# Performance work log

Hardware: AMD Instinct MI355X
Metric: run time of the kernel (lower is better)

Reference implementation:

```python
import jax, jax.numpy as jnp
import numpy as np

N_NODES = 100000


def _gcn_conv(x, W, b, src, dst, deg_inv_sqrt, n):
    # PyG GCNConv: h = x @ W; out[i] = sum_{(j->i)} norm_ji * h[j] + b
    h = x @ W                                   # [N, out_dim]
    norm = deg_inv_sqrt[src] * deg_inv_sqrt[dst]  # [E_total]
    msg = h[src] * norm[:, None]                # gather + scale
    out = jax.ops.segment_sum(msg, dst, num_segments=n)  # scatter-add
    return out + b


def setup_inputs() -> dict:
    key = jax.random.key(0)
    k1, k2, k3, k4, k5, k6 = jax.random.split(key, 6)
    num_features, hidden, embedding_size = 128, 32, 64
    n_edges = 3200000
    x = jax.random.normal(k1, (N_NODES, num_features), dtype=jnp.float32)
    edge_index = jax.random.randint(k2, (2, n_edges), 0, N_NODES, dtype=jnp.int64)
    # Glorot init like PyG GCNConv
    W1 = jax.random.normal(k3, (num_features, hidden), dtype=jnp.float32) * (1.0 / np.sqrt(num_features))
    b1 = jnp.zeros((hidden,), dtype=jnp.float32)
    W2 = jax.random.normal(k4, (hidden, embedding_size), dtype=jnp.float32) * (1.0 / np.sqrt(hidden))
    b2 = jnp.zeros((embedding_size,), dtype=jnp.float32)
    return {"x": x, "edge_index": edge_index, "W1": W1, "b1": b1, "W2": W2, "b2": b2}


def reference(x, edge_index, W1, b1, W2, b2):
    n = x.shape[0]
    # add self-loops (GCNConv default add_self_loops=True)
    loop = jnp.arange(n, dtype=edge_index.dtype)
    src = jnp.concatenate([edge_index[0], loop])
    dst = jnp.concatenate([edge_index[1], loop])
    # symmetric normalization: deg includes self-loops, edge_weight = 1
    deg = jax.ops.segment_sum(jnp.ones_like(dst, dtype=x.dtype), dst, num_segments=n)
    deg_inv_sqrt = jnp.where(deg > 0, jax.lax.rsqrt(deg), 0.0)

    h = _gcn_conv(x, W1, b1, src, dst, deg_inv_sqrt, n)
    h = jax.nn.relu(h)
    # F.dropout(p=0.2, training=False) -> identity in eval mode
    out = _gcn_conv(h, W2, b2, src, dst, deg_inv_sqrt, n)
    return out
```

## Files before the change

kernel.cpp:

```cpp
#include <hip/hip_runtime.h>
#include <hip/hip_bf16.h>


#define NF 128
#define HID 32
#define EMB 64

#define BSHIFT 10
#define BNODES 1024
#define CAP 36864
#define NBUKMAX 128
#define TILE 4096
#define EPT 16
#define CHUNKS 8

typedef float vf4 __attribute__((ext_vector_type(4)));

static __device__ __forceinline__ unsigned bf16rne(float f) {
    unsigned u = __float_as_uint(f);
    return (u + 0x7fffu + ((u >> 16) & 1u)) >> 16;
}

static __device__ __host__ __forceinline__ int hslot(int b, int c) {
    return ((b >> 3) << 6) | (c << 3) | (b & 7);
}

#define ACC8(v) \
    a0 += __uint_as_float((v).x << 16); a1 += __uint_as_float((v).x & 0xffff0000u); \
    a2 += __uint_as_float((v).y << 16); a3 += __uint_as_float((v).y & 0xffff0000u); \
    a4 += __uint_as_float((v).z << 16); a5 += __uint_as_float((v).z & 0xffff0000u); \
    a6 += __uint_as_float((v).w << 16); a7 += __uint_as_float((v).w & 0xffff0000u);

__global__ void k_detect(const unsigned* __restrict__ raw, int* __restrict__ flag) {
    int t = blockIdx.x * blockDim.x + threadIdx.x;
    unsigned w = raw[2 * t + 1];
    if (w != 0u) atomicOr(flag, 1);
}

__global__ __launch_bounds__(256) void k_part(const void* __restrict__ ei,
                                              const int* __restrict__ flag,
                                              unsigned* __restrict__ pairs,
                                              int* __restrict__ bcur,
                                              int* __restrict__ cnt_ovf,
                                              unsigned long long* __restrict__ ovf,
                                              int* __restrict__ ovfcnt,
                                              int E, int nbuk) {
    __shared__ unsigned sEnt[TILE];
    __shared__ unsigned char sB[TILE];
    __shared__ int hcnt[NBUKMAX], lstart[NBUKMAX], gbase[NBUKMAX], lcur[NBUKMAX];
    const int tid = threadIdx.x;
    const int tile0 = blockIdx.x * TILE;
    if (tile0 >= E) return;
    const int tcnt = min(TILE, E - tile0);
    const bool is64 = (*flag == 0);

    for (int b = tid; b < nbuk; b += 256) { hcnt[b] = 0; lcur[b] = 0; }
    __syncthreads();

    int ms[EPT], md[EPT];
#pragma unroll
    for (int k = 0; k < EPT; ++k) {
        int i = tile0 + k * 256 + tid;
        ms[k] = -1;
        if (i < tile0 + tcnt) {
            int s, d;
            if (is64) {
                const long long* p = (const long long*)ei;
                s = (int)__builtin_nontemporal_load(&p[i]);
                d = (int)__builtin_nontemporal_load(&p[(size_t)E + i]);
            } else {
                const int* p = (const int*)ei;
                s = __builtin_nontemporal_load(&p[i]);
                d = __builtin_nontemporal_load(&p[E + i]);
            }
            ms[k] = s; md[k] = d;
            atomicAdd(&hcnt[d >> BSHIFT], 1);
        }
    }
    __syncthreads();

    if (tid < 64) {
        int i0 = tid * 2, i1 = tid * 2 + 1;
        int c0 = (i0 < nbuk) ? hcnt[i0] : 0;
        int c1 = (i1 < nbuk) ? hcnt[i1] : 0;
        int run = c0 + c1, inc = run;
#pragma unroll
        for (int off = 1; off < 64; off <<= 1) {
            int t2 = __shfl_up(inc, off);
            if (tid >= off) inc += t2;
        }
        int excl = inc - run;
        if (i0 < nbuk) { lstart[i0] = excl;      gbase[i0] = c0 ? atomicAdd(&bcur[i0], c0) : 0; }
        if (i1 < nbuk) { lstart[i1] = excl + c0; gbase[i1] = c1 ? atomicAdd(&bcur[i1], c1) : 0; }
    }
    __syncthreads();

#pragma unroll
    for (int k = 0; k < EPT; ++k) {
        if (ms[k] >= 0) {
            int b = md[k] >> BSHIFT;
            int c = atomicAdd(&lcur[b], 1);
            int slot = lstart[b] + c;
            sEnt[slot] = ((unsigned)(md[k] & (BNODES - 1)) << 17) | (unsigned)ms[k];
            sB[slot] = (unsigned char)b;
        }
    }
    __syncthreads();

    for (int j = tid; j < tcnt; j += 256) {
        unsigned ent = sEnt[j];
        int b = sB[j];
        int g = gbase[b] + (j - lstart[b]);
        if (g < CAP) {
            pairs[(size_t)b * CAP + g] = ent;
        } else {
            int d = (b << BSHIFT) | (int)(ent >> 17);
            int s = (int)(ent & 0x1FFFFu);
            int o = atomicAdd(ovfcnt, 1);
            ovf[o] = ((unsigned long long)(unsigned)d << 32) | (unsigned)s;
            atomicAdd(&cnt_ovf[d], 1);
        }
    }
}

__global__ void k_bscan(const int* __restrict__ bcur, int* __restrict__ bbase,
                        int* __restrict__ roff, int nbuk, int E, int N) {
    __shared__ int sh[128];
    int t = threadIdx.x;
    int v = (t < nbuk) ? bcur[t] : 0;
    sh[t] = v;
    __syncthreads();
    for (int off = 1; off < 128; off <<= 1) {
        int add = (t >= off) ? sh[t - off] : 0;
        __syncthreads();
        sh[t] += add;
        __syncthreads();
    }
    if (t < nbuk) bbase[t] = sh[t] - v;
    if (t == 0) roff[N] = E;
}

__global__ __launch_bounds__(256) void k_hist(const unsigned* __restrict__ pairs,
                                              const int* __restrict__ bcur,
                                              int* __restrict__ histc, int nbuk) {
    __shared__ int hist[BNODES];
    const int idx = blockIdx.x;
    const int c = (idx >> 3) & 7;
    const int b = (idx & 7) | ((idx >> 6) << 3);
    if (b >= nbuk) return;
    const int tid = threadIdx.x;
    const int nb = min(bcur[b], CAP);
    const int csz = (nb + CHUNKS - 1) / CHUNKS;
    const int i0 = c * csz, i1 = min(nb, i0 + csz);
    const unsigned* pp = pairs + (size_t)b * CAP;
    for (int i = tid; i < BNODES; i += 256) hist[i] = 0;
    __syncthreads();
    for (int i = i0 + tid; i < i1; i += 256)
        atomicAdd(&hist[__builtin_nontemporal_load(&pp[i]) >> 17], 1);
    __syncthreads();
    int* out = histc + ((size_t)idx << 10);
    for (int i = tid; i < BNODES; i += 256) out[i] = hist[i];
}

__global__ __launch_bounds__(256) void k_nscan(int* __restrict__ histc,
                                               const int* __restrict__ bbase,
                                               const int* __restrict__ cnt_ovf,
                                               int* __restrict__ roff,
                                               int* __restrict__ cursor,
                                               float* __restrict__ dis, int N) {
    __shared__ int part[256];
    const int b = blockIdx.x, tid = threadIdx.x;
    const int base = bbase[b];
    int h[4][CHUNKS], stg[4], tv[4];
    int run = 0;
    const int l0 = tid * 4;
#pragma unroll
    for (int k = 0; k < 4; ++k) {
        int l = l0 + k;
        int node = (b << BSHIFT) + l;
        int st = 0;
#pragma unroll
        for (int c = 0; c < CHUNKS; ++c) {
            h[k][c] = histc[((size_t)hslot(b, c) << 10) + l];
            st += h[k][c];
        }
        stg[k] = st;
        int ov = (node < N) ? cnt_ovf[node] : 0;
        tv[k] = st + ov;
        run += tv[k];
    }
    part[tid] = run;
    __syncthreads();
    for (int off = 1; off < 256; off <<= 1) {
        int add = (tid >= off) ? part[tid - off] : 0;
        __syncthreads();
        part[tid] += add;
        __syncthreads();
    }
    int excl = part[tid] - run;
#pragma unroll
    for (int k = 0; k < 4; ++k) {
        int l = l0 + k;
        int node = (b << BSHIFT) + l;
        if (node < N) {
            roff[node] = base + excl;
            cursor[node] = base + excl + stg[k];
            dis[node] = rsqrtf((float)(tv[k] + 1));
        }
        int cb = base + excl;
#pragma unroll
        for (int c = 0; c < CHUNKS; ++c) {
            int hh = h[k][c];
            histc[((size_t)hslot(b, c) << 10) + l] = cb;
            cb += hh;
        }
        excl += tv[k];
    }
}

__global__ __launch_bounds__(256) void k_scat2(const unsigned* __restrict__ pairs,
                                               const int* __restrict__ bcur,
                                               const int* __restrict__ histc,
                                               int* __restrict__ csr, int nbuk) {
    __shared__ int cbase[BNODES];
    __shared__ int lc[BNODES];
    const int idx = blockIdx.x;
    const int c = (idx >> 3) & 7;
    const int b = (idx & 7) | ((idx >> 6) << 3);
    if (b >= nbuk) return;
    const int tid = threadIdx.x;
    const int nb = min(bcur[b], CAP);
    const int csz = (nb + CHUNKS - 1) / CHUNKS;
    const int i0 = c * csz, i1 = min(nb, i0 + csz);
    const unsigned* pp = pairs + (size_t)b * CAP;
    const int* hc = histc + ((size_t)idx << 10);
    for (int i = tid; i < BNODES; i += 256) { cbase[i] = hc[i]; lc[i] = 0; }
    __syncthreads();
    for (int i = i0 + tid; i < i1; i += 256) {
        unsigned ent = pp[i];
        int l = ent >> 17;
        int pos = cbase[l] + atomicAdd(&lc[l], 1);
        csr[pos] = (int)(ent & 0x1FFFFu);
    }
}

__global__ __launch_bounds__(256) void k_ovf(const unsigned long long* __restrict__ ovf,
                                             const int* __restrict__ ovfcnt,
                                             int* __restrict__ cursor,
                                             int* __restrict__ csr) {
    int n = *ovfcnt;
    for (int i = blockIdx.x * 256 + threadIdx.x; i < n; i += 256 * 8) {
        unsigned long long pr = ovf[i];
        int pos = atomicAdd(&cursor[(int)(unsigned)(pr >> 32)], 1);
        csr[pos] = (int)(unsigned)pr;
    }
}

__global__ __launch_bounds__(256) void k_gemm1(const float* __restrict__ x,
                                               const float* __restrict__ W,
                                               const float* __restrict__ dis,
                                               unsigned* __restrict__ h1b, int N) {
    __shared__ float sW[NF * HID];
    __shared__ float sx[32][132];
    const int t = threadIdx.x;
    for (int i = t; i < NF * HID; i += 256) sW[i] = W[i];
    const int row0 = blockIdx.x * 32;
    {
        const float4* xv = (const float4*)(x + (size_t)row0 * NF);
        for (int i = t; i < 32 * 32; i += 256) {
            int r = i >> 5, c = i & 31;
            float4 v = make_float4(0.f, 0.f, 0.f, 0.f);
            if (row0 + r < N) v = xv[(size_t)r * 32 + c];
            *(float4*)&sx[r][c * 4] = v;
        }
    }
    __syncthreads();
    const int col4 = (t & 7) * 4;
    const int row = t >> 3;
    float a0 = 0.f, a1 = 0.f, a2 = 0.f, a3 = 0.f;
#pragma unroll 8
    for (int k = 0; k < NF; ++k) {
        float xs = sx[row][k];
        float4 w = *(const float4*)&sW[k * HID + col4];
        a0 += xs * w.x; a1 += xs * w.y; a2 += xs * w.z; a3 += xs * w.w;
    }
    int r = row0 + row;
    if (r < N) {
        float d = dis[r];
        unsigned u0 = bf16rne(a0 * d) | (bf16rne(a1 * d) << 16);
        unsigned u1 = bf16rne(a2 * d) | (bf16rne(a3 * d) << 16);
        *(uint2*)&h1b[(size_t)r * 16 + (t & 7) * 2] = make_uint2(u0, u1);
    }
}

__global__ __launch_bounds__(256) void k_agg1(const uint4* __restrict__ h1b,
                                              const int* __restrict__ roff,
                                              const int* __restrict__ csr,
                                              const float* __restrict__ dis,
                                              const float* __restrict__ b1,
                                              uint4* __restrict__ t_out, int N) {
    int tt = blockIdx.x * 256 + threadIdx.x;
    int node = tt >> 2;
    if (node >= N) return;
    int j = tt & 3;
    uint4 u = h1b[(size_t)node * 4 + j];
    float a0, a1, a2, a3, a4, a5, a6, a7;
    a0 = __uint_as_float(u.x << 16); a1 = __uint_as_float(u.x & 0xffff0000u);
    a2 = __uint_as_float(u.y << 16); a3 = __uint_as_float(u.y & 0xffff0000u);
    a4 = __uint_as_float(u.z << 16); a5 = __uint_as_float(u.z & 0xffff0000u);
    a6 = __uint_as_float(u.w << 16); a7 = __uint_as_float(u.w & 0xffff0000u);
    int e0 = roff[node], e1 = roff[node + 1];
    int e = e0;
    for (; e + 4 <= e1; e += 4) {
        int s0 = __builtin_nontemporal_load(&csr[e + 0]);
        int s1 = __builtin_nontemporal_load(&csr[e + 1]);
        int s2 = __builtin_nontemporal_load(&csr[e + 2]);
        int s3 = __builtin_nontemporal_load(&csr[e + 3]);
        uint4 v0 = h1b[(size_t)s0 * 4 + j];
        uint4 v1 = h1b[(size_t)s1 * 4 + j];
        uint4 v2 = h1b[(size_t)s2 * 4 + j];
        uint4 v3 = h1b[(size_t)s3 * 4 + j];
        ACC8(v0) ACC8(v1) ACC8(v2) ACC8(v3)
    }
    for (; e < e1; ++e) {
        int s = __builtin_nontemporal_load(&csr[e]);
        uint4 v = h1b[(size_t)s * 4 + j];
        ACC8(v)
    }
    float d = dis[node];
    float4 bb0 = *(const float4*)&b1[j * 8];
    float4 bb1 = *(const float4*)&b1[j * 8 + 4];
    float r0 = fmaxf(a0 * d + bb0.x, 0.f) * d, r1 = fmaxf(a1 * d + bb0.y, 0.f) * d;
    float r2 = fmaxf(a2 * d + bb0.z, 0.f) * d, r3 = fmaxf(a3 * d + bb0.w, 0.f) * d;
    float r4 = fmaxf(a4 * d + bb1.x, 0.f) * d, r5 = fmaxf(a5 * d + bb1.y, 0.f) * d;
    float r6 = fmaxf(a6 * d + bb1.z, 0.f) * d, r7 = fmaxf(a7 * d + bb1.w, 0.f) * d;
    uint4 o;
    o.x = bf16rne(r0) | (bf16rne(r1) << 16);
    o.y = bf16rne(r2) | (bf16rne(r3) << 16);
    o.z = bf16rne(r4) | (bf16rne(r5) << 16);
    o.w = bf16rne(r6) | (bf16rne(r7) << 16);
    t_out[(size_t)node * 4 + j] = o;
}

__global__ __launch_bounds__(256) void k_agg2(const uint4* __restrict__ tb,
                                              const int* __restrict__ roff,
                                              const int* __restrict__ csr,
                                              const float* __restrict__ dis,
                                              float* __restrict__ s2, int N) {
    int tt = blockIdx.x * 256 + threadIdx.x;
    int node = tt >> 2;
    if (node >= N) return;
    int j = tt & 3;
    uint4 u = tb[(size_t)node * 4 + j];
    float a0, a1, a2, a3, a4, a5, a6, a7;
    a0 = __uint_as_float(u.x << 16); a1 = __uint_as_float(u.x & 0xffff0000u);
    a2 = __uint_as_float(u.y << 16); a3 = __uint_as_float(u.y & 0xffff0000u);
    a4 = __uint_as_float(u.z << 16); a5 = __uint_as_float(u.z & 0xffff0000u);
    a6 = __uint_as_float(u.w << 16); a7 = __uint_as_float(u.w & 0xffff0000u);
    int e0 = roff[node], e1 = roff[node + 1];
    int e = e0;
    for (; e + 4 <= e1; e += 4) {
        int s0 = __builtin_nontemporal_load(&csr[e + 0]);
        int s1 = __builtin_nontemporal_load(&csr[e + 1]);
        int s2i = __builtin_nontemporal_load(&csr[e + 2]);
        int s3 = __builtin_nontemporal_load(&csr[e + 3]);
        uint4 v0 = tb[(size_t)s0 * 4 + j];
        uint4 v1 = tb[(size_t)s1 * 4 + j];
        uint4 v2 = tb[(size_t)s2i * 4 + j];
        uint4 v3 = tb[(size_t)s3 * 4 + j];
        ACC8(v0) ACC8(v1) ACC8(v2) ACC8(v3)
    }
    for (; e < e1; ++e) {
        int s = __builtin_nontemporal_load(&csr[e]);
        uint4 v = tb[(size_t)s * 4 + j];
        ACC8(v)
    }
    float d = dis[node];
    float* op = &s2[(size_t)node * HID + j * 8];
    *(float4*)op       = make_float4(a0 * d, a1 * d, a2 * d, a3 * d);
    *(float4*)(op + 4) = make_float4(a4 * d, a5 * d, a6 * d, a7 * d);
}

__global__ __launch_bounds__(256) void k_gemm2(const float* __restrict__ a,
                                               const float* __restrict__ W,
                                               const float* __restrict__ b2,
                                               float* __restrict__ out, int N) {
    __shared__ float sW[HID * EMB];
    __shared__ float sx[32][36];
    const int t = threadIdx.x;
    for (int i = t; i < HID * EMB; i += 256) sW[i] = W[i];
    const int row0 = blockIdx.x * 32;
    {
        const float4* av = (const float4*)(a + (size_t)row0 * HID);
        int r = t >> 3, c = t & 7;
        float4 v = make_float4(0.f, 0.f, 0.f, 0.f);
        if (row0 + r < N) v = av[(size_t)r * 8 + c];
        *(float4*)&sx[r][c * 4] = v;
    }
    __syncthreads();
    const int col4 = (t & 15) * 4;
    const int r0 = t >> 4;
    float a00 = 0.f, a01 = 0.f, a02 = 0.f, a03 = 0.f;
    float a10 = 0.f, a11 = 0.f, a12 = 0.f, a13 = 0.f;
#pragma unroll
    for (int k = 0; k < HID; ++k) {
        float4 w = *(const float4*)&sW[k * EMB + col4];
        float xa = sx[r0][k];
        float xb = sx[r0 + 16][k];
        a00 += xa * w.x; a01 += xa * w.y; a02 += xa * w.z; a03 += xa * w.w;
        a10 += xb * w.x; a11 += xb * w.y; a12 += xb * w.z; a13 += xb * w.w;
    }
    float4 bb = *(const float4*)&b2[col4];
    int ra = row0 + r0, rb = row0 + r0 + 16;
    if (ra < N) {
        vf4 o; o.x = a00 + bb.x; o.y = a01 + bb.y; o.z = a02 + bb.z; o.w = a03 + bb.w;
        __builtin_nontemporal_store(o, (vf4*)&out[(size_t)ra * EMB + col4]);
    }
    if (rb < N) {
        vf4 o; o.x = a10 + bb.x; o.y = a11 + bb.y; o.z = a12 + bb.z; o.w = a13 + bb.w;
        __builtin_nontemporal_store(o, (vf4*)&out[(size_t)rb * EMB + col4]);
    }
}

extern "C" void kernel_launch(void* const* d_in, const int* in_sizes, int n_in,
                              void* d_out, int out_size, void* d_ws, size_t ws_size,
                              hipStream_t stream) {
    const float* x  = (const float*)d_in[0];
    const void*  ei = d_in[1];
    const float* W1 = (const float*)d_in[2];
    const float* b1 = (const float*)d_in[3];
    const float* W2 = (const float*)d_in[4];
    const float* b2 = (const float*)d_in[5];
    float* out = (float*)d_out;

    const int N = in_sizes[0] / NF;
    const int E = in_sizes[1] / 2;
    const int nbuk = (N + BNODES - 1) >> BSHIFT;

    char* ws = (char*)d_ws;
    size_t off = 0;
    auto take = [&](size_t bytes) -> void* {
        void* p = ws + off;
        off += (bytes + 255) & ~(size_t)255;
        return p;
    };
    int* cnt_ovf = (int*)take((size_t)N * 4);
    int* bcur    = (int*)take((size_t)NBUKMAX * 4);
    int* ovfcnt  = (int*)take(4);
    int* flag    = (int*)take(4);
    size_t zbytes = off;
    int*                bbase  = (int*)take((size_t)NBUKMAX * 4);
    int*                roff   = (int*)take((size_t)(N + 1) * 4);
    int*                cursor = (int*)take((size_t)N * 4);
    float*              dis    = (float*)take((size_t)N * 4);
    int*                histc  = (int*)take((size_t)NBUKMAX * CHUNKS * BNODES * 4);
    unsigned*           pairs  = (unsigned*)take((size_t)nbuk * CAP * 4);
    unsigned long long* ovf    = (unsigned long long*)take((size_t)E * 8);
    int*                csr    = (int*)take((size_t)E * 4);
    unsigned*           h1b    = (unsigned*)take((size_t)N * HID * 2);
    unsigned*           tb     = (unsigned*)take((size_t)N * HID * 2);
    float*              s2     = (float*)take((size_t)N * HID * 4);

    (void)hipMemsetAsync(cnt_ovf, 0, zbytes, stream);

    const int gridBC = ((nbuk + 7) / 8) * 64;

    k_detect<<<16, 256, 0, stream>>>((const unsigned*)ei, flag);
    k_part<<<(E + TILE - 1) / TILE, 256, 0, stream>>>(ei, flag, pairs, bcur, cnt_ovf,
                                                      ovf, ovfcnt, E, nbuk);
    k_bscan<<<1, 128, 0, stream>>>(bcur, bbase, roff, nbuk, E, N);
    k_hist<<<gridBC, 256, 0, stream>>>(pairs, bcur, histc, nbuk);
    k_nscan<<<nbuk, 256, 0, stream>>>(histc, bbase, cnt_ovf, roff, cursor, dis, N);
    k_scat2<<<gridBC, 256, 0, stream>>>(pairs, bcur, histc, csr, nbuk);
    k_ovf<<<8, 256, 0, stream>>>(ovf, ovfcnt, cursor, csr);

    k_gemm1<<<(N + 31) / 32, 256, 0, stream>>>(x, W1, dis, h1b, N);
    k_agg1<<<((size_t)N * 4 + 255) / 256, 256, 0, stream>>>((const uint4*)h1b, roff, csr,
                                                            dis, b1, (uint4*)tb, N);
    k_agg2<<<((size_t)N * 4 + 255) / 256, 256, 0, stream>>>((const uint4*)tb, roff, csr,
                                                            dis, s2, N);
    k_gemm2<<<(N + 31) / 32, 256, 0, stream>>>(s2, W2, b2, out, N);
}
```

Before: 252.5 us.

## Fold dtype detection into partition, per-wave histograms, and unroll gather loops

Removes the separate dtype-detect kernel and does the int32/int64 check inside each partition block. The shared-memory bucket histogram is split per wavefront to reduce atomic contention. The CSR scatter loop is unrolled by four and both aggregation loops by eight to raise memory-level parallelism. The layer-2 aggregation output uses nontemporal stores. The cost is more shared memory and registers, and the detection is now per tile rather than global.

```diff
diff --git a/kernel.cpp b/kernel.cpp
--- a/kernel.cpp
+++ b/kernel.cpp
@@ -15,6 +15,7 @@
 #define CHUNKS 8
 
 typedef float vf4 __attribute__((ext_vector_type(4)));
+typedef unsigned vu4 __attribute__((ext_vector_type(4)));
 
 static __device__ __forceinline__ unsigned bf16rne(float f) {
     unsigned u = __float_as_uint(f);
@@ -31,14 +32,7 @@
     a4 += __uint_as_float((v).z << 16); a5 += __uint_as_float((v).z & 0xffff0000u); \
     a6 += __uint_as_float((v).w << 16); a7 += __uint_as_float((v).w & 0xffff0000u);
 
-__global__ void k_detect(const unsigned* __restrict__ raw, int* __restrict__ flag) {
-    int t = blockIdx.x * blockDim.x + threadIdx.x;
-    unsigned w = raw[2 * t + 1];
-    if (w != 0u) atomicOr(flag, 1);
-}
-
 __global__ __launch_bounds__(256) void k_part(const void* __restrict__ ei,
-                                              const int* __restrict__ flag,
                                               unsigned* __restrict__ pairs,
                                               int* __restrict__ bcur,
                                               int* __restrict__ cnt_ovf,
@@ -47,15 +41,31 @@
                                               int E, int nbuk) {
     __shared__ unsigned sEnt[TILE];
     __shared__ unsigned char sB[TILE];
-    __shared__ int hcnt[NBUKMAX], lstart[NBUKMAX], gbase[NBUKMAX], lcur[NBUKMAX];
+    __shared__ int hcntw[4][NBUKMAX];
+    __shared__ int lcurw[4][NBUKMAX];
+    __shared__ int lstart[NBUKMAX], gbase[NBUKMAX];
+    __shared__ int sNZ;
     const int tid = threadIdx.x;
+    const int w = tid >> 6;
     const int tile0 = blockIdx.x * TILE;
     if (tile0 >= E) return;
     const int tcnt = min(TILE, E - tile0);
-    const bool is64 = (*flag == 0);
-
-    for (int b = tid; b < nbuk; b += 256) { hcnt[b] = 0; lcur[b] = 0; }
-    __syncthreads();
+
+    if (tid == 0) sNZ = 0;
+    for (int b = tid; b < 4 * NBUKMAX; b += 256) {
+        ((int*)hcntw)[b] = 0;
+        ((int*)lcurw)[b] = 0;
+    }
+    __syncthreads();
+    {
+        int i = tile0 + tid;
+        if (i < E) {
+            unsigned hw = ((const unsigned*)ei)[2 * (size_t)i + 1];
+            if (hw) sNZ = 1;
+        }
+    }
+    __syncthreads();
+    const bool is64 = (sNZ == 0);
 
     int ms[EPT], md[EPT];
 #pragma unroll
@@ -74,15 +84,16 @@
                 d = __builtin_nontemporal_load(&p[E + i]);
             }
             ms[k] = s; md[k] = d;
-            atomicAdd(&hcnt[d >> BSHIFT], 1);
+            atomicAdd(&hcntw[w][d >> BSHIFT], 1);
         }
     }
     __syncthreads();
 
     if (tid < 64) {
         int i0 = tid * 2, i1 = tid * 2 + 1;
-        int c0 = (i0 < nbuk) ? hcnt[i0] : 0;
-        int c1 = (i1 < nbuk) ? hcnt[i1] : 0;
+        int c0 = 0, c1 = 0;
+        if (i0 < nbuk) { c0 = hcntw[0][i0] + hcntw[1][i0] + hcntw[2][i0] + hcntw[3][i0]; }
+        if (i1 < nbuk) { c1 = hcntw[0][i1] + hcntw[1][i1] + hcntw[2][i1] + hcntw[3][i1]; }
         int run = c0 + c1, inc = run;
 #pragma unroll
         for (int off = 1; off < 64; off <<= 1) {
@@ -90,8 +101,20 @@
             if (tid >= off) inc += t2;
         }
         int excl = inc - run;
-        if (i0 < nbuk) { lstart[i0] = excl;      gbase[i0] = c0 ? atomicAdd(&bcur[i0], c0) : 0; }
-        if (i1 < nbuk) { lstart[i1] = excl + c0; gbase[i1] = c1 ? atomicAdd(&bcur[i1], c1) : 0; }
+        if (i0 < nbuk) {
+            lstart[i0] = excl;
+            gbase[i0] = c0 ? atomicAdd(&bcur[i0], c0) : 0;
+            int off2 = excl;
+#pragma unroll
+            for (int ww = 0; ww < 4; ++ww) { int t3 = hcntw[ww][i0]; hcntw[ww][i0] = off2; off2 += t3; }
+        }
+        if (i1 < nbuk) {
+            lstart[i1] = excl + c0;
+            gbase[i1] = c1 ? atomicAdd(&bcur[i1], c1) : 0;
+            int off2 = excl + c0;
+#pragma unroll
+            for (int ww = 0; ww < 4; ++ww) { int t3 = hcntw[ww][i1]; hcntw[ww][i1] = off2; off2 += t3; }
+        }
     }
     __syncthreads();
 
@@ -99,8 +122,7 @@
     for (int k = 0; k < EPT; ++k) {
         if (ms[k] >= 0) {
             int b = md[k] >> BSHIFT;
-            int c = atomicAdd(&lcur[b], 1);
-            int slot = lstart[b] + c;
+            int slot = hcntw[w][b] + atomicAdd(&lcurw[w][b], 1);
             sEnt[slot] = ((unsigned)(md[k] & (BNODES - 1)) << 17) | (unsigned)ms[k];
             sB[slot] = (unsigned char)b;
         }
@@ -158,8 +180,8 @@
     for (int i = i0 + tid; i < i1; i += 256)
         atomicAdd(&hist[__builtin_nontemporal_load(&pp[i]) >> 17], 1);
     __syncthreads();
-    int* out = histc + ((size_t)idx << 10);
-    for (int i = tid; i < BNODES; i += 256) out[i] = hist[i];
+    int* outp = histc + ((size_t)idx << 10);
+    for (int i = tid; i < BNODES; i += 256) outp[i] = hist[i];
 }
 
 __global__ __launch_bounds__(256) void k_nscan(int* __restrict__ histc,
@@ -236,7 +258,20 @@
     const int* hc = histc + ((size_t)idx << 10);
     for (int i = tid; i < BNODES; i += 256) { cbase[i] = hc[i]; lc[i] = 0; }
     __syncthreads();
-    for (int i = i0 + tid; i < i1; i += 256) {
+    int i = i0 + tid;
+    for (; i + 768 < i1; i += 1024) {
+        unsigned e0 = pp[i], e1 = pp[i + 256], e2 = pp[i + 512], e3 = pp[i + 768];
+        int l0 = e0 >> 17, l1 = e1 >> 17, l2 = e2 >> 17, l3 = e3 >> 17;
+        int p0 = cbase[l0] + atomicAdd(&lc[l0], 1);
+        int p1 = cbase[l1] + atomicAdd(&lc[l1], 1);
+        int p2 = cbase[l2] + atomicAdd(&lc[l2], 1);
+        int p3 = cbase[l3] + atomicAdd(&lc[l3], 1);
+        csr[p0] = (int)(e0 & 0x1FFFFu);
+        csr[p1] = (int)(e1 & 0x1FFFFu);
+        csr[p2] = (int)(e2 & 0x1FFFFu);
+        csr[p3] = (int)(e3 & 0x1FFFFu);
+    }
+    for (; i < i1; i += 256) {
         unsigned ent = pp[i];
         int l = ent >> 17;
         int pos = cbase[l] + atomicAdd(&lc[l], 1);
@@ -311,6 +346,25 @@
     a6 = __uint_as_float(u.w << 16); a7 = __uint_as_float(u.w & 0xffff0000u);
     int e0 = roff[node], e1 = roff[node + 1];
     int e = e0;
+    for (; e + 8 <= e1; e += 8) {
+        int s0 = __builtin_nontemporal_load(&csr[e + 0]);
+        int s1 = __builtin_nontemporal_load(&csr[e + 1]);
+        int s2 = __builtin_nontemporal_load(&csr[e + 2]);
+        int s3 = __builtin_nontemporal_load(&csr[e + 3]);
+        int s4 = __builtin_nontemporal_load(&csr[e + 4]);
+        int s5 = __builtin_nontemporal_load(&csr[e + 5]);
+        int s6 = __builtin_nontemporal_load(&csr[e + 6]);
+        int s7 = __builtin_nontemporal_load(&csr[e + 7]);
+        uint4 v0 = h1b[(size_t)s0 * 4 + j];
+        uint4 v1 = h1b[(size_t)s1 * 4 + j];
+        uint4 v2 = h1b[(size_t)s2 * 4 + j];
+        uint4 v3 = h1b[(size_t)s3 * 4 + j];
+        uint4 v4 = h1b[(size_t)s4 * 4 + j];
+        uint4 v5 = h1b[(size_t)s5 * 4 + j];
+        uint4 v6 = h1b[(size_t)s6 * 4 + j];
+        uint4 v7 = h1b[(size_t)s7 * 4 + j];
+        ACC8(v0) ACC8(v1) ACC8(v2) ACC8(v3) ACC8(v4) ACC8(v5) ACC8(v6) ACC8(v7)
+    }
     for (; e + 4 <= e1; e += 4) {
         int s0 = __builtin_nontemporal_load(&csr[e + 0]);
         int s1 = __builtin_nontemporal_load(&csr[e + 1]);
@@ -359,6 +413,25 @@
     a6 = __uint_as_float(u.w << 16); a7 = __uint_as_float(u.w & 0xffff0000u);
     int e0 = roff[node], e1 = roff[node + 1];
     int e = e0;
+    for (; e + 8 <= e1; e += 8) {
+        int s0 = __builtin_nontemporal_load(&csr[e + 0]);
+        int s1 = __builtin_nontemporal_load(&csr[e + 1]);
+        int s2i = __builtin_nontemporal_load(&csr[e + 2]);
+        int s3 = __builtin_nontemporal_load(&csr[e + 3]);
+        int s4 = __builtin_nontemporal_load(&csr[e + 4]);
+        int s5 = __builtin_nontemporal_load(&csr[e + 5]);
+        int s6 = __builtin_nontemporal_load(&csr[e + 6]);
+        int s7 = __builtin_nontemporal_load(&csr[e + 7]);
+        uint4 v0 = tb[(size_t)s0 * 4 + j];
+        uint4 v1 = tb[(size_t)s1 * 4 + j];
+        uint4 v2 = tb[(size_t)s2i * 4 + j];
+        uint4 v3 = tb[(size_t)s3 * 4 + j];
+        uint4 v4 = tb[(size_t)s4 * 4 + j];
+        uint4 v5 = tb[(size_t)s5 * 4 + j];
+        uint4 v6 = tb[(size_t)s6 * 4 + j];
+        uint4 v7 = tb[(size_t)s7 * 4 + j];
+        ACC8(v0) ACC8(v1) ACC8(v2) ACC8(v3) ACC8(v4) ACC8(v5) ACC8(v6) ACC8(v7)
+    }
     for (; e + 4 <= e1; e += 4) {
         int s0 = __builtin_nontemporal_load(&csr[e + 0]);
         int s1 = __builtin_nontemporal_load(&csr[e + 1]);
@@ -376,9 +449,12 @@
         ACC8(v)
     }
     float d = dis[node];
-    float* op = &s2[(size_t)node * HID + j * 8];
-    *(float4*)op       = make_float4(a0 * d, a1 * d, a2 * d, a3 * d);
-    *(float4*)(op + 4) = make_float4(a4 * d, a5 * d, a6 * d, a7 * d);
+    vf4 o0, o1;
+    o0.x = a0 * d; o0.y = a1 * d; o0.z = a2 * d; o0.w = a3 * d;
+    o1.x = a4 * d; o1.y = a5 * d; o1.z = a6 * d; o1.w = a7 * d;
+    vf4* op = (vf4*)&s2[(size_t)node * HID + j * 8];
+    __builtin_nontemporal_store(o0, op);
+    __builtin_nontemporal_store(o1, op + 1);
 }
 
 __global__ __launch_bounds__(256) void k_gemm2(const float* __restrict__ a,
@@ -447,7 +523,6 @@
     int* cnt_ovf = (int*)take((size_t)N * 4);
     int* bcur    = (int*)take((size_t)NBUKMAX * 4);
     int* ovfcnt  = (int*)take(4);
-    int* flag    = (int*)take(4);
     size_t zbytes = off;
     int*                bbase  = (int*)take((size_t)NBUKMAX * 4);
     int*                roff   = (int*)take((size_t)(N + 1) * 4);
@@ -464,9 +539,9 @@
     (void)hipMemsetAsync(cnt_ovf, 0, zbytes, stream);
 
     const int gridBC = ((nbuk + 7) / 8) * 64;
-
-    k_detect<<<16, 256, 0, stream>>>((const unsigned*)ei, flag);
-    k_part<<<(E + TILE - 1) / TILE, 256, 0, stream>>>(ei, flag, pairs, bcur, cnt_ovf,
+    const int gridAgg = (int)(((size_t)N * 4 + 255) / 256);
+
+    k_part<<<(E + TILE - 1) / TILE, 256, 0, stream>>>(ei, pairs, bcur, cnt_ovf,
                                                       ovf, ovfcnt, E, nbuk);
     k_bscan<<<1, 128, 0, stream>>>(bcur, bbase, roff, nbuk, E, N);
     k_hist<<<gridBC, 256, 0, stream>>>(pairs, bcur, histc, nbuk);
@@ -475,9 +550,8 @@
     k_ovf<<<8, 256, 0, stream>>>(ovf, ovfcnt, cursor, csr);
 
     k_gemm1<<<(N + 31) / 32, 256, 0, stream>>>(x, W1, dis, h1b, N);
-    k_agg1<<<((size_t)N * 4 + 255) / 256, 256, 0, stream>>>((const uint4*)h1b, roff, csr,
-                                                            dis, b1, (uint4*)tb, N);
-    k_agg2<<<((size_t)N * 4 + 255) / 256, 256, 0, stream>>>((const uint4*)tb, roff, csr,
-                                                            dis, s2, N);
+    k_agg1<<<gridAgg, 256, 0, stream>>>((const uint4*)h1b, roff, csr, dis, b1,
+                                        (uint4*)tb, N);
+    k_agg2<<<gridAgg, 256, 0, stream>>>((const uint4*)tb, roff, csr, dis, s2, N);
     k_gemm2<<<(N + 31) / 32, 256, 0, stream>>>(s2, W2, b2, out, N);
 }
```

Result: faster. 232.5 us (-7.9%).
